# Performance work log

Hardware: AMD Instinct MI355X
Metric: run time of the kernel (lower is better)

## Reference

```python
import jax, jax.numpy as jnp
import numpy as np

R = 4            # sim_radius
K = 2 * R + 1    # 9
NS = K * K       # 81 displacement channels
EPS = 1e-3       # YOLOX BaseConv BN eps


def _conv1x1_bn_silu(x, w, g, b, m, v):
    # x: [B,C,H,W], w: [O,C] -- 1x1 conv (no bias) + BatchNorm(eval) + SiLU
    y = jnp.einsum('bchw,oc->bohw', x, w)
    y = (y - m[:, None, None]) * (g[:, None, None] / jnp.sqrt(v[:, None, None] + EPS)) + b[:, None, None]
    return y * jax.nn.sigmoid(y)


def _resize_bilinear_align(x, Hi, Wi):
    # F.interpolate(mode='bilinear', align_corners=True), separable per axis
    def interp(arr, n_src, n_dst, axis):
        c = jnp.linspace(0.0, n_src - 1.0, n_dst)
        i0 = jnp.floor(c).astype(jnp.int32)
        i1 = jnp.minimum(i0 + 1, n_src - 1)
        wts = (c - i0).astype(arr.dtype)
        sh = [1] * arr.ndim
        sh[axis] = n_dst
        wts = wts.reshape(sh)
        return jnp.take(arr, i0, axis=axis) * (1 - wts) + jnp.take(arr, i1, axis=axis) * wts
    x = interp(x, x.shape[2], Hi, 2)
    x = interp(x, x.shape[3], Wi, 3)
    return x


def setup_inputs():
    key = jax.random.key(0)
    ks = iter(jax.random.split(key, 32))
    B = 4
    chans = (128, 256, 512)
    sizes = ((80, 80), (40, 40), (20, 20))
    hidden = 4
    inp = {}
    for i, (c, (h, w)) in enumerate(zip(chans, sizes)):
        inp[f'features{i}'] = jax.random.normal(next(ks), (B, 4, c, h, w), jnp.float32)
    inp['past_clip_ids'] = jnp.broadcast_to(jnp.arange(-3, 1, dtype=jnp.int32), (B, 4))
    inp['future_clip_ids'] = jnp.ones((B, 1), jnp.int32)
    # sim2_conv_1: 3*81 -> 4
    inp['conv1_w'] = jax.random.normal(next(ks), (hidden, 3 * NS), jnp.float32) * 0.05
    inp['bn1_g'] = jnp.ones((hidden,), jnp.float32)
    inp['bn1_b'] = jnp.zeros((hidden,), jnp.float32)
    inp['bn1_m'] = jax.random.normal(next(ks), (hidden,), jnp.float32) * 0.1
    inp['bn1_v'] = jax.random.uniform(next(ks), (hidden,), jnp.float32, minval=0.5, maxval=1.5)
    # sim2_convs_2: (c+4) -> c per pyramid level
    for i, c in enumerate(chans):
        inp[f'conv2_w{i}'] = jax.random.normal(next(ks), (c, c + hidden), jnp.float32) * (1.0 / np.sqrt(c + hidden))
        inp[f'bn2_g{i}'] = jnp.ones((c,), jnp.float32)
        inp[f'bn2_b{i}'] = jnp.zeros((c,), jnp.float32)
        inp[f'bn2_m{i}'] = jax.random.normal(next(ks), (c,), jnp.float32) * 0.1
        inp[f'bn2_v{i}'] = jax.random.uniform(next(ks), (c,), jnp.float32, minval=0.5, maxval=1.5)
    return inp


def reference(features0, features1, features2,
              conv1_w, bn1_g, bn1_b, bn1_m, bn1_v,
              conv2_w0, bn2_g0, bn2_b0, bn2_m0, bn2_v0,
              conv2_w1, bn2_g1, bn2_b1, bn2_m1, bn2_v1,
              conv2_w2, bn2_g2, bn2_b2, bn2_m2, bn2_v2,
              past_clip_ids, future_clip_ids):
    B, T, C, H, W = features2.shape
    cur = features2[:, -1].reshape(B * C, 1, H, W)
    # identity-kernel F.conv2d == patch extraction (displacement gather for cost volume)
    shifted = jax.lax.conv_general_dilated_patches(
        cur, filter_shape=(K, K), window_strides=(1, 1),
        padding=[(R, R), (R, R)])                      # [B*C, 81, H, W]
    shifted = shifted.reshape(B, 1, C, NS, H, W)
    past = features2[:, :-1][:, :, :, None]            # [B, T-1, C, 1, H, W]
    sim = -jnp.abs(shifted - past)                     # [B, T-1, C, 81, H, W] (dominant intermediate)
    sim = jax.nn.softmax(sim.sum(axis=2), axis=2)      # [B, T-1, 81, H, W], softmax over displacements
    sim = sim.reshape(B, (T - 1) * NS, H, W)
    sim = _conv1x1_bn_silu(sim, conv1_w, bn1_g, bn1_b, bn1_m, bn1_v)  # [B, sim_hidden, H, W]
    feats = (features0, features1, features2)
    p2 = ((conv2_w0, bn2_g0, bn2_b0, bn2_m0, bn2_v0),
          (conv2_w1, bn2_g1, bn2_b1, bn2_m1, bn2_v1),
          (conv2_w2, bn2_g2, bn2_b2, bn2_m2, bn2_v2))
    outs = []
    for f, prm in zip(feats, p2):
        Hi, Wi = f.shape[-2], f.shape[-1]
        p = _resize_bilinear_align(sim, Hi, Wi)
        x = jnp.concatenate([f[:, -1], p], axis=1)     # [B, Ci+hidden, Hi, Wi]
        outs.append(_conv1x1_bn_silu(x, *prm)[:, None])  # [B, 1, Ci, Hi, Wi]
    return tuple(outs)
```

## Files before the change

kernel.cpp:

```cpp
#include <hip/hip_runtime.h>
#include <math.h>

#define EPSBN 1e-3f

#define BB 4
#define TT 4
#define C2 512
#define H2 20
#define W2 20
#define HW2 400
#define RR 4
#define KK 9
#define NS 81
#define NT 3
#define NTS 243
#define HID 4

typedef __attribute__((ext_vector_type(8))) short short8;
typedef __attribute__((ext_vector_type(4))) float floatx4;

static __device__ inline unsigned short f2bf(float f) {
    unsigned int u = __float_as_uint(f);
    unsigned int r = (u + 0x7fffu + ((u >> 16) & 1u)) >> 16;
    return (unsigned short)r;
}

static __device__ inline void prep_frag_body(
    int i,
    const float* __restrict__ w0, const float* __restrict__ w1,
    const float* __restrict__ w2,
    const float* __restrict__ g0, const float* __restrict__ b0,
    const float* __restrict__ m0, const float* __restrict__ v0,
    const float* __restrict__ g1, const float* __restrict__ b1,
    const float* __restrict__ m1, const float* __restrict__ v1,
    const float* __restrict__ g2, const float* __restrict__ b2,
    const float* __restrict__ m2, const float* __restrict__ v2,
    unsigned short* __restrict__ wb0, unsigned short* __restrict__ wb1,
    unsigned short* __restrict__ wb2, float* __restrict__ shift) {
    if (i < 20480) {
        int j = i & 7, lane = (i >> 3) & 63;
        int blk = i >> 9;
        int kb = blk % 5, o16 = blk / 5;
        int o = o16 * 16 + (lane & 15);
        int k = kb * 32 + (lane >> 4) * 8 + j;
        float sc = g0[o] * rsqrtf(v0[o] + EPSBN);
        wb0[i] = f2bf(k < 132 ? w0[o * 132 + k] * sc : 0.f);
        return;
    }
    i -= 20480;
    if (i < 73728) {
        int j = i & 7, lane = (i >> 3) & 63;
        int blk = i >> 9;
        int kb = blk % 9, o16 = blk / 9;
        int o = o16 * 16 + (lane & 15);
        int k = kb * 32 + (lane >> 4) * 8 + j;
        float sc = g1[o] * rsqrtf(v1[o] + EPSBN);
        wb1[i] = f2bf(k < 260 ? w1[o * 260 + k] * sc : 0.f);
        return;
    }
    i -= 73728;
    if (i < 278528) {
        int j = i & 7, lane = (i >> 3) & 63;
        int blk = i >> 9;
        int kb = blk % 17, o16 = blk / 17;
        int o = o16 * 16 + (lane & 15);
        int k = kb * 32 + (lane >> 4) * 8 + j;
        float sc = g2[o] * rsqrtf(v2[o] + EPSBN);
        wb2[i] = f2bf(k < 516 ? w2[o * 516 + k] * sc : 0.f);
        return;
    }
    i -= 278528;
    if (i < 896) {
        if (i < 128) {
            float sc = g0[i] * rsqrtf(v0[i] + EPSBN);
            shift[i] = b0[i] - m0[i] * sc;
        } else if (i < 384) {
            int o = i - 128;
            float sc = g1[o] * rsqrtf(v1[o] + EPSBN);
            shift[i] = b1[o] - m1[o] * sc;
        } else {
            int o = i - 384;
            float sc = g2[o] * rsqrtf(v2[o] + EPSBN);
            shift[i] = b2[o] - m2[o] * sc;
        }
    }
}

static __device__ inline void prep_body(
    int i,
    const float* __restrict__ w0, const float* __restrict__ w1,
    const float* __restrict__ w2,
    const float* __restrict__ g0, const float* __restrict__ b0,
    const float* __restrict__ m0, const float* __restrict__ v0,
    const float* __restrict__ g1, const float* __restrict__ b1,
    const float* __restrict__ m1, const float* __restrict__ v1,
    const float* __restrict__ g2, const float* __restrict__ b2,
    const float* __restrict__ m2, const float* __restrict__ v2,
    unsigned short* __restrict__ wb0, unsigned short* __restrict__ wb1,
    unsigned short* __restrict__ wb2, float* __restrict__ shift) {
    if (i < 128 * 160) {
        int o = i / 160, k = i % 160;
        float sc = g0[o] * rsqrtf(v0[o] + EPSBN);
        wb0[i] = f2bf(k < 132 ? w0[o * 132 + k] * sc : 0.f);
        return;
    }
    i -= 128 * 160;
    if (i < 256 * 288) {
        int o = i / 288, k = i % 288;
        float sc = g1[o] * rsqrtf(v1[o] + EPSBN);
        wb1[i] = f2bf(k < 260 ? w1[o * 260 + k] * sc : 0.f);
        return;
    }
    i -= 256 * 288;
    if (i < 512 * 544) {
        int o = i / 544, k = i % 544;
        float sc = g2[o] * rsqrtf(v2[o] + EPSBN);
        wb2[i] = f2bf(k < 516 ? w2[o * 516 + k] * sc : 0.f);
        return;
    }
    i -= 512 * 544;
    if (i < 896) {
        if (i < 128) {
            float sc = g0[i] * rsqrtf(v0[i] + EPSBN);
            shift[i] = b0[i] - m0[i] * sc;
        } else if (i < 384) {
            int o = i - 128;
            float sc = g1[o] * rsqrtf(v1[o] + EPSBN);
            shift[i] = b1[o] - m1[o] * sc;
        } else {
            int o = i - 384;
            float sc = g2[o] * rsqrtf(v2[o] + EPSBN);
            shift[i] = b2[o] - m2[o] * sc;
        }
    }
}

__global__ void k_prep(const float* w0, const float* w1, const float* w2,
                       const float* g0, const float* b0, const float* m0, const float* v0,
                       const float* g1, const float* b1, const float* m1, const float* v1,
                       const float* g2, const float* b2, const float* m2, const float* v2,
                       unsigned short* wb0, unsigned short* wb1,
                       unsigned short* wb2, float* shift) {
    int i = blockIdx.x * 256 + threadIdx.x;
    prep_body(i, w0, w1, w2, g0, b0, m0, v0, g1, b1, m1, v1, g2, b2, m2, v2,
              wb0, wb1, wb2, shift);
}

__global__ void k_prep_pad(const float* __restrict__ f2, float* __restrict__ pad,
                           const float* w0, const float* w1, const float* w2,
                           const float* g0, const float* b0, const float* m0, const float* v0,
                           const float* g1, const float* b1, const float* m1, const float* v1,
                           const float* g2, const float* b2, const float* m2, const float* v2,
                           unsigned short* wb0, unsigned short* wb1,
                           unsigned short* wb2, float* shift) {
    int bid = blockIdx.x;
    if (bid < 1792) {
        int id = bid * 256 + threadIdx.x;
        if (id >= BB * C2 * 28 * 8) return;
        int c4 = id & 7;
        int tmp = id >> 3;
        int r = tmp % 28;
        int tmp2 = tmp / 28;
        int c = tmp2 % C2;
        int b = tmp2 / C2;
        float4 v = {0.f, 0.f, 0.f, 0.f};
        if (r >= 4 && r < 24 && c4 >= 1 && c4 <= 5)
            v = *(const float4*)(f2 + ((size_t)(b * TT + (TT - 1)) * C2 + c) * HW2 +
                                 (r - 4) * W2 + (c4 - 1) * 4);
        *(float4*)(pad + (size_t)id * 4) = v;
    } else {
        int i = (bid - 1792) * 256 + threadIdx.x;
        prep_frag_body(i, w0, w1, w2, g0, b0, m0, v0, g1, b1, m1, v1, g2, b2, m2, v2,
                       wb0, wb1, wb2, shift);
    }
}

template <int NSPG>
__global__ __launch_bounds__(256) void k_cost_cs(const float* __restrict__ f2,
                                                 const float* __restrict__ pad,
                                                 float* __restrict__ Spart) {
    constexpr int CS = C2 / (NSPG * 2);
    __shared__ float red[36][100];
    int bi = blockIdx.x;
    int cs = bi % NSPG;
    int rem = bi / NSPG;
    int dy = rem % 9; rem /= 9;
    int t = rem % 3;
    int b = rem / 3;
    int tid = threadIdx.x;
    int half = tid >> 7;
    int q = tid & 127;
    bool act = (q < 100);
    int qq = act ? q : 0;
    int h = qq / 5;
    int w0 = (qq % 5) * 4;
    int p = h * W2 + w0;
    int c0 = cs * (2 * CS) + half * CS;

    const float* pr = pad + ((size_t)(b * C2 + c0) * 28 + (h + dy)) * 32 + w0;
    const float* pp = f2 + ((size_t)(b * TT + t) * C2 + c0) * HW2 + p;

    float acc[36];
#pragma unroll
    for (int i = 0; i < 36; ++i) acc[i] = 0.f;

    if (act) {
        float4 ql = *(const float4*)(pr);
        float4 qm = *(const float4*)(pr + 4);
        float4 qr = *(const float4*)(pr + 8);
        float4 pv = *(const float4*)(pp);
        for (int c = 0; c < CS; ++c) {
            float4 nql, nqm, nqr, npv;
            if (c + 1 < CS) {
                pr += 28 * 32;
                pp += HW2;
                nql = *(const float4*)(pr);
                nqm = *(const float4*)(pr + 4);
                nqr = *(const float4*)(pr + 8);
                npv = *(const float4*)(pp);
            }
            float cv[12] = {ql.x, ql.y, ql.z, ql.w,
                            qm.x, qm.y, qm.z, qm.w,
                            qr.x, qr.y, qr.z, qr.w};
#pragma unroll
            for (int dx = 0; dx < 9; ++dx) {
                acc[dx * 4 + 0] += fabsf(cv[dx + 0] - pv.x);
                acc[dx * 4 + 1] += fabsf(cv[dx + 1] - pv.y);
                acc[dx * 4 + 2] += fabsf(cv[dx + 2] - pv.z);
                acc[dx * 4 + 3] += fabsf(cv[dx + 3] - pv.w);
            }
            ql = nql; qm = nqm; qr = nqr; pv = npv;
        }
    }

    if (half == 1 && act) {
#pragma unroll
        for (int i = 0; i < 36; ++i) red[i][qq] = acc[i];
    }
    __syncthreads();
    if (half == 0 && act) {
#pragma unroll
        for (int i = 0; i < 36; ++i) acc[i] += red[i][qq];
#pragma unroll
        for (int px = 0; px < 4; ++px) {
            float* dst = Spart + ((size_t)(cs * BB + b) * HW2 + (p + px)) * 336 +
                         t * 108 + dy * 12;
            float4 u0 = {-acc[0 + px], -acc[4 + px], -acc[8 + px], -acc[12 + px]};
            float4 u1 = {-acc[16 + px], -acc[20 + px], -acc[24 + px], -acc[28 + px]};
            float4 u2 = {-acc[32 + px], 0.f, 0.f, 0.f};
            *(float4*)(dst) = u0;
            *(float4*)(dst + 4) = u1;
            *(float4*)(dst + 8) = u2;
        }
    }
}

template <int NSP, int TS>
__global__ __launch_bounds__(128) void k_cost(const float* __restrict__ f2,
                                              float* __restrict__ Spart) {
    constexpr int CS = C2 / NSP;
    __shared__ float curT[2][28][36];
    int bi = blockIdx.x;
    int cs = bi % NSP;
    int rem = bi / NSP;
    int dy = rem % 9; rem /= 9;
    int t = rem % 3;
    int b = rem / 3;
    int tid = threadIdx.x;
    bool act = (tid < 100);
    int q = act ? tid : 0;
    int h = q / 5;
    int w0 = (q % 5) * 4;
    int p = h * W2 + w0;

    const float* cur = f2 + ((size_t)(b * TT + (TT - 1)) * C2 + cs * CS) * HW2;
    const float* pst = f2 + ((size_t)(b * TT + t) * C2 + cs * CS) * HW2;

    for (int i = tid; i < 2 * 28 * 36; i += 128)
        ((float*)curT)[i] = 0.f;
    __syncthreads();

    float acc[36];
#pragma unroll
    for (int i = 0; i < 36; ++i) acc[i] = 0.f;

    if (act) {
        float4 v = *(const float4*)(cur + p);
        *(float4*)&curT[0][h + 4][w0 + 4] = v;
    }
    __syncthreads();

    for (int c = 0; c < CS; ++c) {
        int buf = c & 1;
        if (act) {
            if (c + 1 < CS) {
                float4 v = *(const float4*)(cur + (size_t)(c + 1) * HW2 + p);
                *(float4*)&curT[buf ^ 1][h + 4][w0 + 4] = v;
            }
            const float* base = &curT[buf][h + dy][w0];
            float4 ql = *(const float4*)(base);
            float4 qm = *(const float4*)(base + 4);
            float4 qr = *(const float4*)(base + 8);
            float4 pv = *(const float4*)(pst + (size_t)c * HW2 + p);
            float cv[12] = {ql.x, ql.y, ql.z, ql.w,
                            qm.x, qm.y, qm.z, qm.w,
                            qr.x, qr.y, qr.z, qr.w};
#pragma unroll
            for (int dx = 0; dx < 9; ++dx) {
                acc[dx * 4 + 0] += fabsf(cv[dx + 0] - pv.x);
                acc[dx * 4 + 1] += fabsf(cv[dx + 1] - pv.y);
                acc[dx * 4 + 2] += fabsf(cv[dx + 2] - pv.z);
                acc[dx * 4 + 3] += fabsf(cv[dx + 3] - pv.w);
            }
        }
        __syncthreads();
    }

    if (act) {
        int tsbase = t * NS + dy * KK;
#pragma unroll
        for (int px = 0; px < 4; ++px) {
            float* dst = Spart + ((size_t)(cs * BB + b) * HW2 + (p + px)) * TS + tsbase;
#pragma unroll
            for (int dx = 0; dx < 9; ++dx) dst[dx] = -acc[dx * 4 + px];
        }
    }
}

template <int NSP, int TS, bool P12>
__global__ __launch_bounds__(256) void k_smax_conv1(
    const float* __restrict__ Spart, const float* __restrict__ w1,
    const float* __restrict__ g1, const float* __restrict__ b1,
    const float* __restrict__ m1, const float* __restrict__ v1,
    float* __restrict__ psim) {
    __shared__ float sS[NTS];
    __shared__ float sP[NTS];
    int bp = blockIdx.x;
    int tid = threadIdx.x;
    if (tid < NTS) {
        int idx;
        if (P12) {
            int t = tid / 81, r = tid % 81;
            idx = t * 108 + (r / 9) * 12 + (r % 9);
        } else {
            idx = tid;
        }
        float S = 0.f;
#pragma unroll
        for (int k = 0; k < NSP; ++k)
            S += Spart[((size_t)(k * BB * HW2) + bp) * TS + idx];
        sS[tid] = S;
    }
    __syncthreads();
    int wave = tid >> 6, lane = tid & 63;
    if (wave < NT) {
        int base = wave * NS;
        float v0 = sS[base + lane];
        float vo = (lane < NS - 64) ? sS[base + 64 + lane] : -1e30f;
        float m = fmaxf(v0, vo);
#pragma unroll
        for (int off = 32; off; off >>= 1) m = fmaxf(m, __shfl_xor(m, off));
        float e0 = __expf(v0 - m);
        float e1 = (lane < NS - 64) ? __expf(vo - m) : 0.f;
        float s = e0 + e1;
#pragma unroll
        for (int off = 32; off; off >>= 1) s += __shfl_xor(s, off);
        float inv = 1.f / s;
        sP[base + lane] = e0 * inv;
        if (lane < NS - 64) sP[base + 64 + lane] = e1 * inv;
    }
    __syncthreads();
    if (tid < 64) {
        int o = tid >> 4, j = tid & 15;
        float acc = 0.f;
#pragma unroll
        for (int mm = 0; mm < 16; ++mm) {
            int k = j + (mm << 4);
            if (k < NTS) acc += w1[o * NTS + k] * sP[k];
        }
#pragma unroll
        for (int off = 8; off; off >>= 1) acc += __shfl_xor(acc, off);
        if (j == 0) {
            float sc = g1[o] * rsqrtf(v1[o] + EPSBN);
            float y = (acc - m1[o]) * sc + b1[o];
            float sig = 1.f / (1.f + __expf(-y));
            psim[(size_t)bp * HID + o] = y * sig;
        }
    }
}

__global__ void k_resize(const float* __restrict__ psim, float* __restrict__ pre0,
                         float* __restrict__ pre1) {
    int id = blockIdx.x * 256 + threadIdx.x;
    int Hi, Wi, bb2, pp;
    float* dst;
    if (id < BB * 6400) {
        Hi = 80; Wi = 80; bb2 = id / 6400; pp = id % 6400; dst = pre0 + (size_t)id * 4;
    } else {
        id -= BB * 6400;
        if (id >= BB * 1600) return;
        Hi = 40; Wi = 40; bb2 = id / 1600; pp = id % 1600; dst = pre1 + (size_t)id * 4;
    }
    int yi = pp / Wi, xi = pp % Wi;
    float cy = yi * (19.0f / (Hi - 1));
    float cx = xi * (19.0f / (Wi - 1));
    int y0 = (int)cy; if (y0 > 19) y0 = 19;
    int x0 = (int)cx; if (x0 > 19) x0 = 19;
    int y1 = min(y0 + 1, 19);
    int x1 = min(x0 + 1, 19);
    float wy = cy - y0, wx = cx - x0;
    const float4* base = (const float4*)psim + (size_t)bb2 * HW2;
    float4 v00 = base[y0 * 20 + x0];
    float4 v01 = base[y0 * 20 + x1];
    float4 v10 = base[y1 * 20 + x0];
    float4 v11 = base[y1 * 20 + x1];
    float4 r0, r1, o4;
    r0.x = v00.x * (1.f - wy) + v10.x * wy; r0.y = v00.y * (1.f - wy) + v10.y * wy;
    r0.z = v00.z * (1.f - wy) + v10.z * wy; r0.w = v00.w * (1.f - wy) + v10.w * wy;
    r1.x = v01.x * (1.f - wy) + v11.x * wy; r1.y = v01.y * (1.f - wy) + v11.y * wy;
    r1.z = v01.z * (1.f - wy) + v11.z * wy; r1.w = v01.w * (1.f - wy) + v11.w * wy;
    o4.x = r0.x * (1.f - wx) + r1.x * wx; o4.y = r0.y * (1.f - wx) + r1.y * wx;
    o4.z = r0.z * (1.f - wx) + r1.z * wx; o4.w = r0.w * (1.f - wx) + r1.w * wx;
    *(float4*)dst = o4;
}

template <int HI, int WI>
static __device__ inline float bil(const float* __restrict__ psim, int b, int p, int ch) {
    int yi = p / WI, xi = p % WI;
    float cy = yi * (19.0f / (HI - 1));
    float cx = xi * (19.0f / (WI - 1));
    int y0 = (int)cy; if (y0 > 19) y0 = 19;
    int x0 = (int)cx; if (x0 > 19) x0 = 19;
    int y1 = min(y0 + 1, 19);
    int x1 = min(x0 + 1, 19);
    float wy = cy - y0, wx = cx - x0;
    const float* base = psim + (size_t)b * HW2 * 4;
    float v00 = base[(y0 * 20 + x0) * 4 + ch];
    float v01 = base[(y0 * 20 + x1) * 4 + ch];
    float v10 = base[(y1 * 20 + x0) * 4 + ch];
    float v11 = base[(y1 * 20 + x1) * 4 + ch];
    float r0 = v00 * (1.f - wy) + v10 * wy;
    float r1 = v01 * (1.f - wy) + v11 * wy;
    return r0 * (1.f - wx) + r1 * wx;
}

template <int CI, int K, int KP, int HW, int TILES, int HI, int WI>
static __device__ inline void pack_body(int cid, const float* __restrict__ f,
                                        const float* __restrict__ psim,
                                        unsigned short* __restrict__ xp) {
    constexpr int KB = KP / 32;
    int tid = threadIdx.x;
    int b = cid / (TILES * KB);
    int rem = cid % (TILES * KB);
    int tile = rem / KB;
    int ks = rem % KB;
    int px = tid >> 2;
    int p = tile * 64 + px;
    int c0 = ks * 32 + (tid & 3) * 8;
    bool pok = (p < HW);
    const float* fb = f + ((size_t)(b * TT + (TT - 1)) * CI) * HW + p;

    short8 o;
#pragma unroll
    for (int j = 0; j < 8; ++j) {
        int c = c0 + j;
        float v = 0.f;
        if (pok) {
            if (c < CI) v = fb[(size_t)c * HW];
            else if (c < K) v = bil<HI, WI>(psim, b, p, c - CI);
        }
        o[j] = (short)f2bf(v);
    }
    ((short8*)(xp + ((size_t)(b * TILES + tile) * KB + ks) * 2048))[tid] = o;
}

__global__ __launch_bounds__(256) void k_pack(
    const float* __restrict__ f0, const float* __restrict__ f1,
    const float* __restrict__ f2, const float* __restrict__ psim,
    unsigned short* __restrict__ xp0, unsigned short* __restrict__ xp1,
    unsigned short* __restrict__ xp2) {
    int bid = blockIdx.x;
    if (bid < 2000) {
        pack_body<128, 132, 160, 6400, 100, 80, 80>(bid, f0, psim, xp0);
    } else if (bid < 2900) {
        pack_body<256, 260, 288, 1600, 25, 40, 40>(bid - 2000, f1, psim, xp1);
    } else {
        pack_body<512, 516, 544, 400, 7, 20, 20>(bid - 2900, f2, psim, xp2);
    }
}

template <int O, int KP, int HW, int TILES>
static __device__ inline void gemmP_body(int lbid, const unsigned short* __restrict__ xp,
                                         const unsigned short* __restrict__ wbF,
                                         const float* __restrict__ shift,
                                         float* __restrict__ out,
                                         unsigned short* __restrict__ xls,
                                         float* __restrict__ cls_all) {
    constexpr int OB = O / 64;
    constexpr int KB = KP / 32;

    int tid = threadIdx.x;
    int lane = tid & 63, wv = tid >> 6;
    int ob = lbid % OB;
    int rest = lbid / OB;
    int b = rest / TILES;
    int tile = rest % TILES;
    int p0 = tile * 64;

    int l15 = lane & 15, lhi = lane >> 4;
    int o_w = ob * 64 + (wv & 1) * 32;
    int pw_loc = (wv >> 1) * 32;

    int o16 = o_w >> 4;
    const short8* a0p = (const short8*)wbF + ((size_t)o16 * KB) * 64 + lane;
    const short8* a1p = a0p + (size_t)KB * 64;
    const short8* chunk = (const short8*)(xp + ((size_t)(b * TILES + tile) * KB) * 2048);

    floatx4 acc00 = {0.f, 0.f, 0.f, 0.f}, acc01 = acc00, acc10 = acc00, acc11 = acc00;

    short8 v = chunk[tid];
    ((short8*)xls)[tid] = v;
    if (KB > 1) v = chunk[256 + tid];
    __syncthreads();

    for (int ks = 0; ks < KB; ++ks) {
        const unsigned short* buf = xls + (ks & 1) * 2048;
        short8 cb0 = *(const short8*)&buf[(pw_loc + l15) * 32 + lhi * 8];
        short8 cb1 = *(const short8*)&buf[(pw_loc + 16 + l15) * 32 + lhi * 8];
        if (ks + 1 < KB) {
            ((short8*)(xls + ((ks + 1) & 1) * 2048))[tid] = v;
            if (ks + 2 < KB) v = chunk[(ks + 2) * 256 + tid];
        }
        short8 ca0 = a0p[ks * 64];
        short8 ca1 = a1p[ks * 64];
        acc00 = __builtin_amdgcn_mfma_f32_16x16x32_bf16(ca0, cb0, acc00, 0, 0, 0);
        acc01 = __builtin_amdgcn_mfma_f32_16x16x32_bf16(ca0, cb1, acc01, 0, 0, 0);
        acc10 = __builtin_amdgcn_mfma_f32_16x16x32_bf16(ca1, cb0, acc10, 0, 0, 0);
        acc11 = __builtin_amdgcn_mfma_f32_16x16x32_bf16(ca1, cb1, acc11, 0, 0, 0);
        __syncthreads();
    }

    float* cls = cls_all + wv * (32 * 36);
#pragma unroll
    for (int osub = 0; osub < 2; ++osub) {
#pragma unroll
        for (int psub = 0; psub < 2; ++psub) {
            floatx4 d = osub ? (psub ? acc11 : acc10) : (psub ? acc01 : acc00);
#pragma unroll
            for (int r = 0; r < 4; ++r)
                cls[(osub * 16 + lhi * 4 + r) * 36 + psub * 16 + l15] = d[r];
        }
    }
#pragma unroll
    for (int i = 0; i < 4; ++i) {
        int o_loc = (lane >> 3) + i * 8;
        int pq = (lane & 7) * 4;
        int p = p0 + pw_loc + pq;
        if (p < HW) {
            float4 vv = *(float4*)&cls[o_loc * 36 + pq];
            int o = o_w + o_loc;
            float sh = shift[o];
            float4 so;
            float y;
            y = vv.x + sh; so.x = y / (1.f + __expf(-y));
            y = vv.y + sh; so.y = y / (1.f + __expf(-y));
            y = vv.z + sh; so.z = y / (1.f + __expf(-y));
            y = vv.w + sh; so.w = y / (1.f + __expf(-y));
            *(float4*)&out[((size_t)b * O + o) * HW + p] = so;
        }
    }
}

__global__ __launch_bounds__(256) void k_gemmP_all(
    const unsigned short* __restrict__ xp0, const unsigned short* __restrict__ xp1,
    const unsigned short* __restrict__ xp2,
    const unsigned short* __restrict__ wb0, const unsigned short* __restrict__ wb1,
    const unsigned short* __restrict__ wb2,
    const float* __restrict__ shift, float* __restrict__ out) {
    __shared__ unsigned short xls[4096];
    __shared__ float cls[4 * 32 * 36];
    int bid = blockIdx.x;
    if (bid < 800) {
        gemmP_body<128, 160, 6400, 100>(bid, xp0, wb0, shift, out, xls, cls);
    } else if (bid < 1200) {
        gemmP_body<256, 288, 1600, 25>(bid - 800, xp1, wb1, shift + 128,
                                       out + 3276800, xls, cls);
    } else {
        gemmP_body<512, 544, 400, 7>(bid - 1200, xp2, wb2, shift + 384,
                                     out + 3276800 + 1638400, xls, cls);
    }
}

#define XLS_STRIDE 40
template <int O, int KP, int K, int HW, int TILES>
__global__ __launch_bounds__(256) void k_gemm(
    const float* __restrict__ f, const float* __restrict__ pre,
    const unsigned short* __restrict__ wb, const float* __restrict__ shift,
    float* __restrict__ out) {
    constexpr int CI = O;
    constexpr int OB = O / 64;
    __shared__ unsigned short xlsf[64 * XLS_STRIDE];

    int tid = threadIdx.x;
    int lane = tid & 63, wv = tid >> 6;
    int ob = blockIdx.x % OB;
    int rest = blockIdx.x / OB;
    int b = rest / TILES;
    int p0 = (rest % TILES) * 64;

    int l15 = lane & 15, lhi = lane >> 4;
    int o_w = ob * 64 + (wv & 1) * 32;
    int pw_loc = (wv >> 1) * 32;

    int c_l = tid >> 3;
    int pq = (tid & 7) * 8;
    const float* fbase = f + ((size_t)(b * TT + (TT - 1)) * CI) * HW;
    const float* pbase = pre + (size_t)b * HW * 4;

    const short8* aptr0 = (const short8*)(wb + (size_t)(o_w + l15) * KP + lhi * 8);
    const short8* aptr1 = (const short8*)(wb + (size_t)(o_w + 16 + l15) * KP + lhi * 8);

    floatx4 acc00 = {0.f, 0.f, 0.f, 0.f}, acc01 = acc00, acc10 = acc00, acc11 = acc00;

    for (int c0 = 0; c0 < KP; c0 += 32) {
        __syncthreads();
        {
            int c = c0 + c_l;
            float vals[8];
            if (c < CI) {
                const float* src = fbase + (size_t)c * HW + p0 + pq;
                if (p0 + pq + 7 < HW) {
                    float4 a = ((const float4*)src)[0];
                    float4 bq = ((const float4*)src)[1];
                    vals[0] = a.x; vals[1] = a.y; vals[2] = a.z; vals[3] = a.w;
                    vals[4] = bq.x; vals[5] = bq.y; vals[6] = bq.z; vals[7] = bq.w;
                } else {
#pragma unroll
                    for (int i = 0; i < 8; ++i) {
                        int p = p0 + pq + i;
                        vals[i] = (p < HW) ? src[i] : 0.f;
                    }
                }
            } else if (c < K) {
#pragma unroll
                for (int i = 0; i < 8; ++i) {
                    int p = p0 + pq + i;
                    vals[i] = (p < HW) ? pbase[(size_t)p * 4 + (c - CI)] : 0.f;
                }
            } else {
#pragma unroll
                for (int i = 0; i < 8; ++i) vals[i] = 0.f;
            }
#pragma unroll
            for (int i = 0; i < 8; ++i)
                xlsf[(pq + i) * XLS_STRIDE + c_l] = f2bf(vals[i]);
        }
        __syncthreads();

        short8 ca0 = aptr0[c0 >> 3];
        short8 ca1 = aptr1[c0 >> 3];
        short8 cb0 = *(const short8*)&xlsf[(pw_loc + l15) * XLS_STRIDE + lhi * 8];
        short8 cb1 = *(const short8*)&xlsf[(pw_loc + 16 + l15) * XLS_STRIDE + lhi * 8];
        acc00 = __builtin_amdgcn_mfma_f32_16x16x32_bf16(ca0, cb0, acc00, 0, 0, 0);
        acc01 = __builtin_amdgcn_mfma_f32_16x16x32_bf16(ca0, cb1, acc01, 0, 0, 0);
        acc10 = __builtin_amdgcn_mfma_f32_16x16x32_bf16(ca1, cb0, acc10, 0, 0, 0);
        acc11 = __builtin_amdgcn_mfma_f32_16x16x32_bf16(ca1, cb1, acc11, 0, 0, 0);
    }

#pragma unroll
    for (int osub = 0; osub < 2; ++osub) {
#pragma unroll
        for (int psub = 0; psub < 2; ++psub) {
            floatx4 d = osub ? (psub ? acc11 : acc10) : (psub ? acc01 : acc00);
            int p = p0 + pw_loc + psub * 16 + l15;
            int obase = o_w + osub * 16 + lhi * 4;
            if (p < HW) {
#pragma unroll
                for (int r = 0; r < 4; ++r) {
                    int o = obase + r;
                    float y = d[r] + shift[o];
                    float sig = 1.f / (1.f + __expf(-y));
                    out[((size_t)b * O + o) * HW + p] = y * sig;
                }
            }
        }
    }
}

extern "C" void kernel_launch(void* const* d_in, const int* in_sizes, int n_in,
                              void* d_out, int out_size, void* d_ws, size_t ws_size,
                              hipStream_t stream) {
    const float* f0 = (const float*)d_in[0];
    const float* f1 = (const float*)d_in[1];
    const float* f2 = (const float*)d_in[2];
    const float* w1 = (const float*)d_in[5];
    const float* g1 = (const float*)d_in[6];
    const float* b1 = (const float*)d_in[7];
    const float* m1 = (const float*)d_in[8];
    const float* v1 = (const float*)d_in[9];
    const float* w2_0 = (const float*)d_in[10];
    const float* g2_0 = (const float*)d_in[11];
    const float* b2_0 = (const float*)d_in[12];
    const float* m2_0 = (const float*)d_in[13];
    const float* v2_0 = (const float*)d_in[14];
    const float* w2_1 = (const float*)d_in[15];
    const float* g2_1 = (const float*)d_in[16];
    const float* b2_1 = (const float*)d_in[17];
    const float* m2_1 = (const float*)d_in[18];
    const float* v2_1 = (const float*)d_in[19];
    const float* w2_2 = (const float*)d_in[20];
    const float* g2_2 = (const float*)d_in[21];
    const float* b2_2 = (const float*)d_in[22];
    const float* m2_2 = (const float*)d_in[23];
    const float* v2_2 = (const float*)d_in[24];

    float* ws = (float*)d_ws;
    const size_t PADSZ = (size_t)BB * C2 * 28 * 32;
    const size_t SP336_8 = (size_t)8 * BB * HW2 * 336;
    const size_t SP8 = (size_t)8 * BB * HW2 * 256;
    const size_t XP0 = 2048000, XP1 = 921600, XP2 = 487424;
    const size_t need2 =
        (SP336_8 + PADSZ + 6400 + 10240 + 36864 + 139264 + 896 + XP0 + XP1 + XP2) * 4;
    int mode = (ws_size >= need2) ? 2 : 0;

    float* out = (float*)d_out;

    if (mode == 2) {
        float* Spart = ws;
        float* pad = ws + SP336_8;
        float* psim = pad + PADSZ;
        unsigned short* wb0 = (unsigned short*)(psim + 6400);
        unsigned short* wb1 = wb0 + 20480;
        unsigned short* wb2 = wb1 + 73728;
        float* shift = (float*)(wb2 + 278528);
        float* xb = shift + 896;
        unsigned short* xp0 = (unsigned short*)xb;
        unsigned short* xp1 = (unsigned short*)(xb + XP0);
        unsigned short* xp2 = (unsigned short*)(xb + XP0 + XP1);

        k_prep_pad<<<dim3(3252), dim3(256), 0, stream>>>(
            f2, pad,
            w2_0, w2_1, w2_2,
            g2_0, b2_0, m2_0, v2_0,
            g2_1, b2_1, m2_1, v2_1,
            g2_2, b2_2, m2_2, v2_2,
            wb0, wb1, wb2, shift);
        k_cost_cs<8><<<dim3(8 * 108), dim3(256), 0, stream>>>(f2, pad, Spart);
        k_smax_conv1<8, 336, true><<<dim3(1600), dim3(256), 0, stream>>>(
            Spart, w1, g1, b1, m1, v1, psim);
        k_pack<<<dim3(3376), dim3(256), 0, stream>>>(f0, f1, f2, psim, xp0, xp1, xp2);
        k_gemmP_all<<<dim3(1424), dim3(256), 0, stream>>>(
            xp0, xp1, xp2, wb0, wb1, wb2, shift, out);
    } else {
        float* Spart = ws;
        float* psim = ws + SP8;
        float* pre0 = psim + 6400;
        float* pre1 = pre0 + 102400;
        unsigned short* wb0 = (unsigned short*)(pre1 + 25600);
        unsigned short* wb1 = wb0 + 20480;
        unsigned short* wb2 = wb1 + 73728;
        float* shift = (float*)(wb2 + 278528);

        k_prep<<<dim3(1460), dim3(256), 0, stream>>>(
            w2_0, w2_1, w2_2,
            g2_0, b2_0, m2_0, v2_0,
            g2_1, b2_1, m2_1, v2_1,
            g2_2, b2_2, m2_2, v2_2,
            wb0, wb1, wb2, shift);
        k_cost<8, 256><<<dim3(8 * 108), dim3(128), 0, stream>>>(f2, Spart);
        k_smax_conv1<8, 256, false><<<dim3(1600), dim3(256), 0, stream>>>(
            Spart, w1, g1, b1, m1, v1, psim);
        k_resize<<<dim3(125), dim3(256), 0, stream>>>(psim, pre0, pre1);
        k_gemm<128, 160, 132, 6400, 100><<<dim3(800), dim3(256), 0, stream>>>(
            f0, pre0, wb0, shift, out);
        k_gemm<256, 288, 260, 1600, 25><<<dim3(400), dim3(256), 0, stream>>>(
            f1, pre1, wb1, shift + 128, out + 3276800);
        k_gemm<512, 544, 516, 400, 7><<<dim3(224), dim3(256), 0, stream>>>(
            f2, psim, wb2, shift + 384, out + 3276800 + 1638400);
    }
}
```

Measured before the change: 65.33 us.

## Pack feature channels alongside cost kernel, pack sim channels in separate small kernel

The bf16 packing of raw feature channels, which does not depend on the similarity result, moves into the cost-volume kernel's launch as extra blocks so it overlaps with the cost computation. Only the four interpolated similarity channels are written afterward by a small dedicated kernel. This takes the large feature-pack pass off the critical path after the softmax/conv1 step. In exchange, the fused launch has heterogeneous blocks with different shared-memory needs, which may affect occupancy. The sim-pack kernel writes only the four sim entries of each last K-slice; the zero padding beyond them relies on pack_f_body having already written zeros there.

```diff
diff --git a/kernel.cpp b/kernel.cpp
--- a/kernel.cpp
+++ b/kernel.cpp
@@ -176,12 +176,11 @@
 }
 
 template <int NSPG>
-__global__ __launch_bounds__(256) void k_cost_cs(const float* __restrict__ f2,
-                                                 const float* __restrict__ pad,
-                                                 float* __restrict__ Spart) {
+static __device__ inline void cost_cs_body(int bi, const float* __restrict__ f2,
+                                           const float* __restrict__ pad,
+                                           float* __restrict__ Spart) {
     constexpr int CS = C2 / (NSPG * 2);
     __shared__ float red[36][100];
-    int bi = blockIdx.x;
     int cs = bi % NSPG;
     int rem = bi / NSPG;
     int dy = rem % 9; rem /= 9;
@@ -253,6 +252,107 @@
             *(float4*)(dst + 8) = u2;
         }
     }
+}
+
+template <int CI, int KP, int HW, int TILES>
+static __device__ inline void pack_f_body(int cid, const float* __restrict__ f,
+                                          unsigned short* __restrict__ xp) {
+    constexpr int KB = KP / 32;
+    int tid = threadIdx.x;
+    int b = cid / (TILES * KB);
+    int rem = cid % (TILES * KB);
+    int tile = rem / KB;
+    int ks = rem % KB;
+    int px = tid >> 2;
+    int p = tile * 64 + px;
+    int c0 = ks * 32 + (tid & 3) * 8;
+    bool pok = (p < HW);
+    const float* fb = f + ((size_t)(b * TT + (TT - 1)) * CI) * HW + p;
+
+    short8 o;
+#pragma unroll
+    for (int j = 0; j < 8; ++j) {
+        int c = c0 + j;
+        float v = 0.f;
+        if (pok && c < CI) v = fb[(size_t)c * HW];
+        o[j] = (short)f2bf(v);
+    }
+    ((short8*)(xp + ((size_t)(b * TILES + tile) * KB + ks) * 2048))[tid] = o;
+}
+
+__global__ __launch_bounds__(256) void k_cost_packf(
+    const float* __restrict__ f2, const float* __restrict__ pad,
+    float* __restrict__ Spart,
+    const float* __restrict__ f0, const float* __restrict__ f1,
+    unsigned short* __restrict__ xp0, unsigned short* __restrict__ xp1,
+    unsigned short* __restrict__ xp2) {
+    int bid = blockIdx.x;
+    if (bid < 864) {
+        cost_cs_body<8>(bid, f2, pad, Spart);
+    } else {
+        int pb = bid - 864;
+        if (pb < 2000) {
+            pack_f_body<128, 160, 6400, 100>(pb, f0, xp0);
+        } else if (pb < 2900) {
+            pack_f_body<256, 288, 1600, 25>(pb - 2000, f1, xp1);
+        } else {
+            pack_f_body<512, 544, 400, 7>(pb - 2900, f2, xp2);
+        }
+    }
+}
+
+template <int HI, int WI>
+static __device__ inline float bil(const float* __restrict__ psim, int b, int p, int ch) {
+    int yi = p / WI, xi = p % WI;
+    float cy = yi * (19.0f / (HI - 1));
+    float cx = xi * (19.0f / (WI - 1));
+    int y0 = (int)cy; if (y0 > 19) y0 = 19;
+    int x0 = (int)cx; if (x0 > 19) x0 = 19;
+    int y1 = min(y0 + 1, 19);
+    int x1 = min(x0 + 1, 19);
+    float wy = cy - y0, wx = cx - x0;
+    const float* base = psim + (size_t)b * HW2 * 4;
+    float v00 = base[(y0 * 20 + x0) * 4 + ch];
+    float v01 = base[(y0 * 20 + x1) * 4 + ch];
+    float v10 = base[(y1 * 20 + x0) * 4 + ch];
+    float v11 = base[(y1 * 20 + x1) * 4 + ch];
+    float r0 = v00 * (1.f - wy) + v10 * wy;
+    float r1 = v01 * (1.f - wy) + v11 * wy;
+    return r0 * (1.f - wx) + r1 * wx;
+}
+
+template <int CI, int KP, int HW, int TILES, int HI, int WI>
+static __device__ inline void pack_sim_body(int id, const float* __restrict__ psim,
+                                            unsigned short* __restrict__ xp) {
+    constexpr int KB = KP / 32;
+    constexpr int KS = CI / 32;
+    int b = id / HW, p = id % HW;
+    int tile = p / 64, px = p % 64;
+    unsigned int lo = (unsigned int)f2bf(bil<HI, WI>(psim, b, p, 0)) |
+                      ((unsigned int)f2bf(bil<HI, WI>(psim, b, p, 1)) << 16);
+    unsigned int hi = (unsigned int)f2bf(bil<HI, WI>(psim, b, p, 2)) |
+                      ((unsigned int)f2bf(bil<HI, WI>(psim, b, p, 3)) << 16);
+    uint2 u = {lo, hi};
+    *(uint2*)(xp + ((size_t)(b * TILES + tile) * KB + KS) * 2048 + px * 32) = u;
+}
+
+__global__ __launch_bounds__(256) void k_pack_sim(
+    const float* __restrict__ psim,
+    unsigned short* __restrict__ xp0, unsigned short* __restrict__ xp1,
+    unsigned short* __restrict__ xp2) {
+    int id = blockIdx.x * 256 + threadIdx.x;
+    if (id < 25600) {
+        pack_sim_body<128, 160, 6400, 100, 80, 80>(id, psim, xp0);
+        return;
+    }
+    id -= 25600;
+    if (id < 6400) {
+        pack_sim_body<256, 288, 1600, 25, 40, 40>(id, psim, xp1);
+        return;
+    }
+    id -= 6400;
+    if (id < 1600)
+        pack_sim_body<512, 544, 400, 7, 20, 20>(id, psim, xp2);
 }
 
 template <int NSP, int TS>
@@ -422,71 +522,6 @@
     o4.x = r0.x * (1.f - wx) + r1.x * wx; o4.y = r0.y * (1.f - wx) + r1.y * wx;
     o4.z = r0.z * (1.f - wx) + r1.z * wx; o4.w = r0.w * (1.f - wx) + r1.w * wx;
     *(float4*)dst = o4;
-}
-
-template <int HI, int WI>
-static __device__ inline float bil(const float* __restrict__ psim, int b, int p, int ch) {
-    int yi = p / WI, xi = p % WI;
-    float cy = yi * (19.0f / (HI - 1));
-    float cx = xi * (19.0f / (WI - 1));
-    int y0 = (int)cy; if (y0 > 19) y0 = 19;
-    int x0 = (int)cx; if (x0 > 19) x0 = 19;
-    int y1 = min(y0 + 1, 19);
-    int x1 = min(x0 + 1, 19);
-    float wy = cy - y0, wx = cx - x0;
-    const float* base = psim + (size_t)b * HW2 * 4;
-    float v00 = base[(y0 * 20 + x0) * 4 + ch];
-    float v01 = base[(y0 * 20 + x1) * 4 + ch];
-    float v10 = base[(y1 * 20 + x0) * 4 + ch];
-    float v11 = base[(y1 * 20 + x1) * 4 + ch];
-    float r0 = v00 * (1.f - wy) + v10 * wy;
-    float r1 = v01 * (1.f - wy) + v11 * wy;
-    return r0 * (1.f - wx) + r1 * wx;
-}
-
-template <int CI, int K, int KP, int HW, int TILES, int HI, int WI>
-static __device__ inline void pack_body(int cid, const float* __restrict__ f,
-                                        const float* __restrict__ psim,
-                                        unsigned short* __restrict__ xp) {
-    constexpr int KB = KP / 32;
-    int tid = threadIdx.x;
-    int b = cid / (TILES * KB);
-    int rem = cid % (TILES * KB);
-    int tile = rem / KB;
-    int ks = rem % KB;
-    int px = tid >> 2;
-    int p = tile * 64 + px;
-    int c0 = ks * 32 + (tid & 3) * 8;
-    bool pok = (p < HW);
-    const float* fb = f + ((size_t)(b * TT + (TT - 1)) * CI) * HW + p;
-
-    short8 o;
-#pragma unroll
-    for (int j = 0; j < 8; ++j) {
-        int c = c0 + j;
-        float v = 0.f;
-        if (pok) {
-            if (c < CI) v = fb[(size_t)c * HW];
-            else if (c < K) v = bil<HI, WI>(psim, b, p, c - CI);
-        }
-        o[j] = (short)f2bf(v);
-    }
-    ((short8*)(xp + ((size_t)(b * TILES + tile) * KB + ks) * 2048))[tid] = o;
-}
-
-__global__ __launch_bounds__(256) void k_pack(
-    const float* __restrict__ f0, const float* __restrict__ f1,
-    const float* __restrict__ f2, const float* __restrict__ psim,
-    unsigned short* __restrict__ xp0, unsigned short* __restrict__ xp1,
-    unsigned short* __restrict__ xp2) {
-    int bid = blockIdx.x;
-    if (bid < 2000) {
-        pack_body<128, 132, 160, 6400, 100, 80, 80>(bid, f0, psim, xp0);
-    } else if (bid < 2900) {
-        pack_body<256, 260, 288, 1600, 25, 40, 40>(bid - 2000, f1, psim, xp1);
-    } else {
-        pack_body<512, 516, 544, 400, 7, 20, 20>(bid - 2900, f2, psim, xp2);
-    }
 }
 
 template <int O, int KP, int HW, int TILES>
@@ -745,10 +780,11 @@
             g2_1, b2_1, m2_1, v2_1,
             g2_2, b2_2, m2_2, v2_2,
             wb0, wb1, wb2, shift);
-        k_cost_cs<8><<<dim3(8 * 108), dim3(256), 0, stream>>>(f2, pad, Spart);
+        k_cost_packf<<<dim3(4240), dim3(256), 0, stream>>>(
+            f2, pad, Spart, f0, f1, xp0, xp1, xp2);
         k_smax_conv1<8, 336, true><<<dim3(1600), dim3(256), 0, stream>>>(
             Spart, w1, g1, b1, m1, v1, psim);
-        k_pack<<<dim3(3376), dim3(256), 0, stream>>>(f0, f1, f2, psim, xp0, xp1, xp2);
+        k_pack_sim<<<dim3(132), dim3(256), 0, stream>>>(psim, xp0, xp1, xp2);
         k_gemmP_all<<<dim3(1424), dim3(256), 0, stream>>>(
             xp0, xp1, xp2, wb0, wb1, wb2, shift, out);
     } else {
```

After: 60.65 us, median of 2. 7.2% less time.
